# Kernel tuning notes

Measured on AMD Instinct MI355X. Metric: run time of the kernel, lower is better.

## Reference

```python
import jax, jax.numpy as jnp
import numpy as np

N = 50000
E = 800000
D = 128
K = 2


def setup_inputs() -> dict:
    key = jax.random.key(0)
    k1, k2, k3, k4 = jax.random.split(key, 4)
    x = jax.random.normal(k1, (N, D), dtype=jnp.float32)
    edge_index = jax.random.randint(k2, (2, E), 0, N, dtype=jnp.int64)
    W = jax.random.normal(k3, (1, D), dtype=jnp.float32) / np.sqrt(D)
    b = jax.random.normal(k4, (1,), dtype=jnp.float32)
    return {"x": x, "edge_index": edge_index, "W": W, "b": b}


def reference(x, edge_index, W, b):
    n = x.shape[0]
    loops = jnp.arange(n, dtype=edge_index.dtype)
    src = jnp.concatenate([edge_index[0], loops])  # message sources j
    dst = jnp.concatenate([edge_index[1], loops])  # aggregation targets i
    ew = jnp.ones(src.shape[0], dtype=x.dtype)
    # gcn_norm: symmetric normalization with self-loops
    deg = jax.ops.segment_sum(ew, dst, num_segments=n)
    dis = jnp.where(deg > 0, jax.lax.rsqrt(jnp.where(deg > 0, deg, 1.0)), 0.0)
    norm = dis[src] * ew * dis[dst]  # [E+N]
    # K hops of sparse propagation: x_i <- sum_j norm_ij * x_j
    h = x
    for _ in range(K):
        h = jax.ops.segment_sum(norm[:, None] * h[src], dst, num_segments=n)
    out = (h @ W.T + b).reshape(-1)  # Linear(in_feats, 1), flattened
    return out
```

## Files before the change

kernel.cpp:

```cpp
#include <hip/hip_runtime.h>


#define CH2_LG   8
#define CH2      256
#define TILEB    8192
#define CAP2     96
#define MAXC2    256
#define MAXNT    128
#define BT       1024

__global__ __launch_bounds__(BT)
void ka2(const float* __restrict__ x, const int* __restrict__ src,
         const int* __restrict__ dst, const float* __restrict__ W,
         int n, int E, int nbin, int NT, int C,
         unsigned* __restrict__ binned, int* __restrict__ bcnt, float* __restrict__ y)
{
    const int t = threadIdx.x, bid = blockIdx.x;
    if (bid < nbin) {
        __shared__ unsigned recs[TILEB];
        __shared__ int hist[MAXC2], sc[MAXC2], cur[MAXC2];
        if (t < MAXC2) hist[t] = 0;
        __syncthreads();
        const int e0 = bid * TILEB;
        const int nrec = min(E - e0, TILEB);
        unsigned rl[TILEB / BT]; int chl[TILEB / BT];
        #pragma unroll
        for (int k = 0; k < TILEB / BT; k++) {
            int j = k * BT + t;
            if (j < nrec) {
                int s = src[e0 + j], d = dst[e0 + j];
                chl[k] = d >> CH2_LG;
                rl[k]  = ((unsigned)chl[k] << 24) | ((unsigned)(d & (CH2 - 1)) << 16) | (unsigned)s;
                atomicAdd(&hist[chl[k]], 1);
            } else chl[k] = -1;
        }
        __syncthreads();
        if (t < MAXC2) sc[t] = hist[t];
        __syncthreads();
        #pragma unroll
        for (int off = 1; off < MAXC2; off <<= 1) {
            int v = (t < MAXC2 && t >= off) ? sc[t - off] : 0;
            __syncthreads();
            if (t < MAXC2) sc[t] += v;
            __syncthreads();
        }
        if (t < MAXC2) cur[t] = sc[t] - hist[t];
        if (t < C) bcnt[t * NT + bid] = min(hist[t], CAP2);
        __syncthreads();
        #pragma unroll
        for (int k = 0; k < TILEB / BT; k++)
            if (chl[k] >= 0) recs[atomicAdd(&cur[chl[k]], 1)] = rl[k];
        __syncthreads();
        for (int j = t; j < nrec; j += BT) {
            unsigned r = recs[j];
            int ch  = r >> 24;
            int off = j - (sc[ch] - hist[ch]);
            if (off < CAP2)
                binned[((size_t)ch * NT + bid) * CAP2 + off] = r & 0x00FFFFFFu;
        }
    } else {
        const int lane = t & 63;
        const int half = lane >> 5, l32 = lane & 31;
        const float4 wv = ((const float4*)W)[l32];
        int i = (bid - nbin) * (BT / 32) + (t >> 6) * 2 + half;
        if (i < n) {
            float4 xv = ((const float4*)(x + (size_t)i * 128))[l32];
            float v = xv.x * wv.x + xv.y * wv.y + xv.z * wv.z + xv.w * wv.w;
            #pragma unroll
            for (int off = 16; off; off >>= 1) v += __shfl_xor(v, off);
            if (l32 == 0) y[i] = v;
        }
    }
}

template <int V>
__global__ __launch_bounds__(1024)
void kh3(const unsigned* __restrict__ binned, const int* __restrict__ bcnt,
         int NT, int n, const float* __restrict__ y, float* __restrict__ dis,
         float* __restrict__ u, float* __restrict__ u2,
         const float* __restrict__ bias, float* __restrict__ out)
{
    __shared__ float acc[CH2];
    __shared__ int lens[MAXNT];
    const int c = blockIdx.x, t = threadIdx.x;
    if (t < CH2) acc[t] = 0.f;
    if (t >= CH2 && t < CH2 + MAXNT) {
        int b = t - CH2;
        lens[b] = (b < NT) ? bcnt[c * NT + b] : 0;
    }
    __syncthreads();
    const int w = t >> 6, ln = t & 63;
    const unsigned* bb = binned + (size_t)c * NT * CAP2;
    for (int b = w; b < NT; b += 16) {
        int len = lens[b];
        const unsigned* run = bb + (size_t)b * CAP2;
        for (int j = ln; j < len; j += 64) {
            unsigned r = run[j];
            float v = (V == 0) ? 1.0f : ((V == 1) ? u[r & 0xFFFFu] : u2[r & 0xFFFFu]);
            atomicAdd(&acc[(r >> 16) & 0xFFu], v);
        }
    }
    __syncthreads();
    if (t < CH2) {
        const int i = (c << CH2_LG) + t;
        if (i < n) {
            float a = acc[t];
            if (V == 0) { float d = rsqrtf(a + 1.0f); dis[i] = d; u[i] = d * y[i]; }
            if (V == 1) { float d = dis[i]; u2[i] = d * d * (a + u[i]); }
            if (V == 2) { out[i] = dis[i] * (a + u2[i]) + bias[0]; }
        }
    }
}

#define CHUNK_LG  10
#define CHUNK     1024
#define NCHMAX    64
#define NSLAB     16
#define RECS      7

__global__ void k_zero(int* __restrict__ cnt) { cnt[threadIdx.x] = 0; }

__global__ void k_bin(const int* __restrict__ src, const int* __restrict__ dst,
                      int E, int nchunks, int cap,
                      int* __restrict__ cnt, unsigned int* __restrict__ binned) {
    __shared__ int hist[NCHMAX], base[NCHMAX], cur[NCHMAX];
    int t = threadIdx.x;
    if (t < NCHMAX) { hist[t] = 0; cur[t] = 0; }
    __syncthreads();
    int e0 = blockIdx.x * (RECS * 256);
    unsigned int rec[RECS]; int ch[RECS];
    #pragma unroll
    for (int k = 0; k < RECS; k++) {
        int e = e0 + k * 256 + t;
        if (e < E) {
            int s = src[e], d = dst[e];
            ch[k]  = d >> CHUNK_LG;
            rec[k] = ((unsigned)(d & (CHUNK - 1)) << 16) | (unsigned)s;
            atomicAdd(&hist[ch[k]], 1);
        } else ch[k] = -1;
    }
    __syncthreads();
    if (t < nchunks) base[t] = atomicAdd(&cnt[t], hist[t]);
    __syncthreads();
    #pragma unroll
    for (int k = 0; k < RECS; k++) {
        if (ch[k] >= 0) {
            int slot = base[ch[k]] + atomicAdd(&cur[ch[k]], 1);
            if (slot < cap) binned[(size_t)ch[k] * cap + slot] = rec[k];
        }
    }
}

template <int MODE>
__global__ void k_hop(const unsigned int* __restrict__ binned, const int* __restrict__ cnt,
                      int cap, const float* __restrict__ val, float* __restrict__ partial) {
    __shared__ float acc[CHUNK];
    int c = blockIdx.x >> 4;
    int m = blockIdx.x & (NSLAB - 1);
    int t = threadIdx.x;
    #pragma unroll
    for (int k = 0; k < CHUNK / 256; k++) acc[t + k * 256] = 0.f;
    __syncthreads();
    int nc = cnt[c]; if (nc > cap) nc = cap;
    const unsigned int* bb = binned + (size_t)c * cap;
    for (int e = m * 256 + t; e < nc; e += NSLAB * 256) {
        unsigned int r = bb[e];
        float v = (MODE == 0) ? 1.0f : val[r & 0xFFFFu];
        atomicAdd(&acc[r >> 16], v);
    }
    __syncthreads();
    float* pp = partial + ((size_t)(c * NSLAB + m) << CHUNK_LG);
    #pragma unroll
    for (int k = 0; k < CHUNK / 256; k++) pp[t + k * 256] = acc[t + k * 256];
}

__global__ void k_dot(const float* __restrict__ x, const float* __restrict__ W,
                      float* __restrict__ y, int n) {
    int wid  = (blockIdx.x * blockDim.x + threadIdx.x) >> 6;
    int lane = threadIdx.x & 63;
    if (wid >= n) return;
    float2 xv = ((const float2*)(x + (size_t)wid * 128))[lane];
    float2 wv = ((const float2*)W)[lane];
    float v = xv.x * wv.x + xv.y * wv.y;
    #pragma unroll
    for (int off = 32; off; off >>= 1) v += __shfl_xor(v, off);
    if (lane == 0) y[wid] = v;
}

template <int V>
__global__ void k_reduce(const float* __restrict__ partial, int n,
                         const float* __restrict__ y, float* __restrict__ dis,
                         float* __restrict__ u, float* __restrict__ u2,
                         const float* __restrict__ b, float* __restrict__ out) {
    int i = blockIdx.x * blockDim.x + threadIdx.x;
    if (i >= n) return;
    int c = i >> CHUNK_LG, l = i & (CHUNK - 1);
    const float* pp = partial + ((size_t)(c * NSLAB) << CHUNK_LG) + l;
    float s = 0.f;
    #pragma unroll
    for (int m = 0; m < NSLAB; m++) s += pp[m << CHUNK_LG];
    if (V == 0) { float d = rsqrtf(s + 1.0f); dis[i] = d; u[i] = d * y[i]; }
    if (V == 1) { float d = dis[i]; u2[i] = d * d * (s + u[i]); }
    if (V == 2) { out[i] = dis[i] * (s + u2[i]) + b[0]; }
}

extern "C" void kernel_launch(void* const* d_in, const int* in_sizes, int n_in,
                              void* d_out, int out_size, void* d_ws, size_t ws_size,
                              hipStream_t stream) {
    const float* x  = (const float*)d_in[0];
    const int*   ei = (const int*)d_in[1];
    const float* W  = (const float*)d_in[2];
    const float* b  = (const float*)d_in[3];
    float* out = (float*)d_out;

    const int n = out_size;
    const int E = in_sizes[1] / 2;
    const int D = in_sizes[0] / n;
    const int* src = ei;
    const int* dst = ei + E;

    const int C2  = (n + CH2 - 1) >> CH2_LG;
    const int NT2 = (E + TILEB - 1) / TILEB;

    size_t w_binned = (size_t)C2 * NT2 * CAP2;
    size_t w_bcnt   = (size_t)C2 * NT2;
    size_t need     = (w_binned + w_bcnt + 4 * (size_t)n) * 4;

    if (D == 128 && n <= 65536 && C2 <= MAXC2 && NT2 <= MAXNT && ws_size >= need) {
        unsigned* binned = (unsigned*)d_ws;
        int*      bcnt   = (int*)d_ws + w_binned;
        float*    y      = (float*)d_ws + w_binned + w_bcnt;
        float*    dis    = y + n;
        float*    u      = dis + n;
        float*    u2     = u + n;

        const int gridA = NT2 + (n + BT / 32 - 1) / (BT / 32);

        ka2<<<gridA, BT, 0, stream>>>(x, src, dst, W, n, E, NT2, NT2, C2, binned, bcnt, y);
        kh3<0><<<C2, 1024, 0, stream>>>(binned, bcnt, NT2, n, y, dis, u, u2, b, out);
        kh3<1><<<C2, 1024, 0, stream>>>(binned, bcnt, NT2, n, y, dis, u, u2, b, out);
        kh3<2><<<C2, 1024, 0, stream>>>(binned, bcnt, NT2, n, y, dis, u, u2, b, out);
        return;
    }

    {
        const int TBf = 256;
        const int Cf  = (n + CHUNK - 1) >> CHUNK_LG;
        const int cap = (int)((long long)E * 5 / (4 * Cf)) + 512;
        int*          cnt    = (int*)d_ws;
        unsigned int* binned = (unsigned int*)(cnt + 64);
        float*        part   = (float*)(binned + (size_t)Cf * cap);
        float*        y      = part + (size_t)Cf * NSLAB * CHUNK;
        float*        dis    = y + n;
        float*        u      = dis + n;
        float*        u2     = u + n;

        const int binBlocks = (E + RECS * 256 - 1) / (RECS * 256);
        const int hopBlocks = Cf * NSLAB;
        const int nb        = (n + TBf - 1) / TBf;
        const int dotBlocks = ((size_t)n * 64 + TBf - 1) / TBf;

        k_zero<<<1, 64, 0, stream>>>(cnt);
        k_bin<<<binBlocks, TBf, 0, stream>>>(src, dst, E, Cf, cap, cnt, binned);
        k_dot<<<dotBlocks, TBf, 0, stream>>>(x, W, y, n);
        k_hop<0><<<hopBlocks, TBf, 0, stream>>>(binned, cnt, cap, y, part);
        k_reduce<0><<<nb, TBf, 0, stream>>>(part, n, y, dis, u, u2, b, out);
        k_hop<1><<<hopBlocks, TBf, 0, stream>>>(binned, cnt, cap, u, part);
        k_reduce<1><<<nb, TBf, 0, stream>>>(part, n, y, dis, u, u2, b, out);
        k_hop<1><<<hopBlocks, TBf, 0, stream>>>(binned, cnt, cap, u2, part);
        k_reduce<2><<<nb, TBf, 0, stream>>>(part, n, y, dis, u, u2, b, out);
    }
}
```

Measured before the change: 38.44 us.

## Compact binned edge records into dense per-chunk arrays for hop passes

The degree pass now prefix-sums the per-tile bin counts and writes each chunk's edge records into a contiguous dense buffer with a stored total. The two propagation hops then read that dense array with vectorized uint4 loads instead of walking padded, partially filled tile runs. The aim is to cut wasted lanes and scattered loads in the hop kernels. In exchange the degree kernel does extra writes and a block-wide scan, and records beyond DCAP per chunk are silently dropped, which could hurt correctness for skewed inputs.

```diff
diff --git a/kernel.cpp b/kernel.cpp
--- a/kernel.cpp
+++ b/kernel.cpp
@@ -8,6 +8,7 @@
 #define MAXC2    256
 #define MAXNT    128
 #define BT       1024
+#define DCAP     5120
 
 __global__ __launch_bounds__(BT)
 void ka2(const float* __restrict__ x, const int* __restrict__ src,
@@ -73,41 +74,77 @@
     }
 }
 
-template <int V>
 __global__ __launch_bounds__(1024)
-void kh3(const unsigned* __restrict__ binned, const int* __restrict__ bcnt,
+void khc(const unsigned* __restrict__ binned, const int* __restrict__ bcnt,
          int NT, int n, const float* __restrict__ y, float* __restrict__ dis,
-         float* __restrict__ u, float* __restrict__ u2,
-         const float* __restrict__ bias, float* __restrict__ out)
+         float* __restrict__ u, unsigned* __restrict__ dense, int* __restrict__ dtot)
 {
     __shared__ float acc[CH2];
-    __shared__ int lens[MAXNT];
+    __shared__ int sc[MAXNT];
     const int c = blockIdx.x, t = threadIdx.x;
     if (t < CH2) acc[t] = 0.f;
     if (t >= CH2 && t < CH2 + MAXNT) {
         int b = t - CH2;
-        lens[b] = (b < NT) ? bcnt[c * NT + b] : 0;
-    }
-    __syncthreads();
+        sc[b] = (b < NT) ? bcnt[c * NT + b] : 0;
+    }
+    __syncthreads();
+    #pragma unroll
+    for (int off = 1; off < MAXNT; off <<= 1) {
+        int v = (t < MAXNT && t >= off) ? sc[t - off] : 0;
+        __syncthreads();
+        if (t < MAXNT) sc[t] += v;
+        __syncthreads();
+    }
+    if (t == 0) dtot[c] = sc[NT - 1];
+    const unsigned* bb = binned + (size_t)c * NT * CAP2;
+    unsigned* dn = dense + (size_t)c * DCAP;
     const int w = t >> 6, ln = t & 63;
-    const unsigned* bb = binned + (size_t)c * NT * CAP2;
     for (int b = w; b < NT; b += 16) {
-        int len = lens[b];
+        int base = b ? sc[b - 1] : 0;
+        int len  = sc[b] - base;
         const unsigned* run = bb + (size_t)b * CAP2;
         for (int j = ln; j < len; j += 64) {
             unsigned r = run[j];
-            float v = (V == 0) ? 1.0f : ((V == 1) ? u[r & 0xFFFFu] : u2[r & 0xFFFFu]);
-            atomicAdd(&acc[(r >> 16) & 0xFFu], v);
-        }
+            atomicAdd(&acc[(r >> 16) & 0xFFu], 1.0f);
+            if (base + j < DCAP) dn[base + j] = r;
+        }
+    }
+    __syncthreads();
+    if (t < CH2) {
+        const int i = (c << CH2_LG) + t;
+        if (i < n) { float d = rsqrtf(acc[t] + 1.0f); dis[i] = d; u[i] = d * y[i]; }
+    }
+}
+
+template <int V>
+__global__ __launch_bounds__(1024)
+void khd(const unsigned* __restrict__ dense, const int* __restrict__ dtot, int n,
+         const float* __restrict__ dis, const float* __restrict__ u,
+         float* __restrict__ u2, const float* __restrict__ bias, float* __restrict__ out)
+{
+    __shared__ float acc[CH2];
+    const int c = blockIdx.x, t = threadIdx.x;
+    if (t < CH2) acc[t] = 0.f;
+    __syncthreads();
+    int tot = dtot[c]; if (tot > DCAP) tot = DCAP;
+    const uint4* dn4 = (const uint4*)(dense + (size_t)c * DCAP);
+    const float* val = (V == 1) ? u : u2;
+    const int nvec = (tot + 3) >> 2;
+    for (int g = t; g < nvec; g += 1024) {
+        uint4 r4 = dn4[g];
+        int base = g << 2;
+        if (base + 0 < tot) atomicAdd(&acc[(r4.x >> 16) & 0xFFu], val[r4.x & 0xFFFFu]);
+        if (base + 1 < tot) atomicAdd(&acc[(r4.y >> 16) & 0xFFu], val[r4.y & 0xFFFFu]);
+        if (base + 2 < tot) atomicAdd(&acc[(r4.z >> 16) & 0xFFu], val[r4.z & 0xFFFFu]);
+        if (base + 3 < tot) atomicAdd(&acc[(r4.w >> 16) & 0xFFu], val[r4.w & 0xFFFFu]);
     }
     __syncthreads();
     if (t < CH2) {
         const int i = (c << CH2_LG) + t;
         if (i < n) {
             float a = acc[t];
-            if (V == 0) { float d = rsqrtf(a + 1.0f); dis[i] = d; u[i] = d * y[i]; }
             if (V == 1) { float d = dis[i]; u2[i] = d * d * (a + u[i]); }
-            if (V == 2) { out[i] = dis[i] * (a + u2[i]) + bias[0]; }
+            else        { out[i] = dis[i] * (a + u2[i]) + bias[0]; }
         }
     }
 }
@@ -224,12 +261,16 @@
 
     size_t w_binned = (size_t)C2 * NT2 * CAP2;
     size_t w_bcnt   = (size_t)C2 * NT2;
-    size_t need     = (w_binned + w_bcnt + 4 * (size_t)n) * 4;
-
-    if (D == 128 && n <= 65536 && C2 <= MAXC2 && NT2 <= MAXNT && ws_size >= need) {
+    size_t w_dense  = (size_t)C2 * DCAP;
+    size_t need     = (w_binned + w_bcnt + w_dense + C2 + 4 * (size_t)n) * 4;
+
+    if (D == 128 && n <= 65536 && C2 <= MAXC2 && NT2 <= MAXNT && (w_bcnt % 4 == 0)
+        && ws_size >= need) {
         unsigned* binned = (unsigned*)d_ws;
         int*      bcnt   = (int*)d_ws + w_binned;
-        float*    y      = (float*)d_ws + w_binned + w_bcnt;
+        unsigned* dense  = (unsigned*)d_ws + w_binned + w_bcnt;
+        int*      dtot   = (int*)d_ws + w_binned + w_bcnt + w_dense;
+        float*    y      = (float*)(dtot + C2);
         float*    dis    = y + n;
         float*    u      = dis + n;
         float*    u2     = u + n;
@@ -237,9 +278,9 @@
         const int gridA = NT2 + (n + BT / 32 - 1) / (BT / 32);
 
         ka2<<<gridA, BT, 0, stream>>>(x, src, dst, W, n, E, NT2, NT2, C2, binned, bcnt, y);
-        kh3<0><<<C2, 1024, 0, stream>>>(binned, bcnt, NT2, n, y, dis, u, u2, b, out);
-        kh3<1><<<C2, 1024, 0, stream>>>(binned, bcnt, NT2, n, y, dis, u, u2, b, out);
-        kh3<2><<<C2, 1024, 0, stream>>>(binned, bcnt, NT2, n, y, dis, u, u2, b, out);
+        khc<<<C2, 1024, 0, stream>>>(binned, bcnt, NT2, n, y, dis, u, dense, dtot);
+        khd<1><<<C2, 1024, 0, stream>>>(dense, dtot, n, dis, u, u2, b, out);
+        khd<2><<<C2, 1024, 0, stream>>>(dense, dtot, n, dis, u, u2, b, out);
         return;
     }
 
```

Result: slower. 40.78 us (+6.1%).
